# Performance work log

Hardware: AMD Instinct MI355X
Metric: run time of the kernel (lower is better)

The kernel has to match this reference:

```python
import jax, jax.numpy as jnp
import numpy as np
from jax import lax

B, S, I, H, NC = 64, 512, 512, 1024, 2


def _lstm_layer(x, w_ih, w_hh, b_ih, b_hh):
    """x: [B,S,Iin] -> hs: [B,S,H]. PyTorch gate order: i, f, g, o."""
    Bx = x.shape[0]
    Hh = w_hh.shape[1]
    b = b_ih + b_hh
    # Precompute input contribution for all timesteps: [S,B,4H]
    xg = jnp.einsum('bsi,gi->sbg', x, w_ih) + b

    def step(carry, xg_t):
        h, c = carry
        gates = xg_t + h @ w_hh.T  # [B,4H]
        i, f, g, o = jnp.split(gates, 4, axis=-1)
        i = jax.nn.sigmoid(i)
        f = jax.nn.sigmoid(f)
        g = jnp.tanh(g)
        o = jax.nn.sigmoid(o)
        c = f * c + i * g
        h = o * jnp.tanh(c)
        return (h, c), h

    h0 = jnp.zeros((Bx, Hh), x.dtype)
    c0 = jnp.zeros((Bx, Hh), x.dtype)
    (_, _), hs = lax.scan(step, (h0, c0), xg)
    return jnp.transpose(hs, (1, 0, 2))  # [B,S,H]


def setup_inputs() -> dict:
    key = jax.random.key(0)
    ks = jax.random.split(key, 11)
    s_i = 1.0 / np.sqrt(H)
    return {
        'x': jax.random.normal(ks[0], (B, S, I), jnp.float32),
        'w_ih0': jax.random.uniform(ks[1], (4 * H, I), jnp.float32, -s_i, s_i),
        'w_hh0': jax.random.uniform(ks[2], (4 * H, H), jnp.float32, -s_i, s_i),
        'b_ih0': jax.random.uniform(ks[3], (4 * H,), jnp.float32, -s_i, s_i),
        'b_hh0': jax.random.uniform(ks[4], (4 * H,), jnp.float32, -s_i, s_i),
        'w_ih1': jax.random.uniform(ks[5], (4 * H, H), jnp.float32, -s_i, s_i),
        'w_hh1': jax.random.uniform(ks[6], (4 * H, H), jnp.float32, -s_i, s_i),
        'b_ih1': jax.random.uniform(ks[7], (4 * H,), jnp.float32, -s_i, s_i),
        'b_hh1': jax.random.uniform(ks[8], (4 * H,), jnp.float32, -s_i, s_i),
        'fc_w': jax.random.uniform(ks[9], (NC, H), jnp.float32, -s_i, s_i),
        'fc_b': jax.random.uniform(ks[10], (NC,), jnp.float32, -s_i, s_i),
    }


def reference(x, w_ih0, w_hh0, b_ih0, b_hh0, w_ih1, w_hh1, b_ih1, b_hh1, fc_w, fc_b):
    # dropout p=0.0 -> identity (eval semantics)
    h = _lstm_layer(x, w_ih0, w_hh0, b_ih0, b_hh0)
    h = _lstm_layer(h, w_ih1, w_hh1, b_ih1, b_hh1)
    last = h[:, -1, :]  # [B,H]
    logits = last @ fc_w.T + fc_b  # [B,NC]
    return jax.nn.softmax(logits, axis=1)
```

## Files before the change

### kernel.cpp

```cpp
#include <hip/hip_runtime.h>

typedef __attribute__((ext_vector_type(8))) short short8;
typedef __attribute__((ext_vector_type(4))) float f32x4;
typedef __attribute__((ext_vector_type(2))) unsigned int u32x2;
typedef unsigned short u16;
typedef unsigned int u32;

#define XB_OFF 0ul
#define H0_OFF 33554432ul
#define H1_OFF 100794368ul
#define FL_OFF 168034304ul
#define FLAGS_LEN 32768ul

#define LDS_TOTAL 131072

__device__ __forceinline__ u16 f2bf(float f) {
  u32 u = __float_as_uint(f);
  return (u16)((u + 0x7fffu + ((u >> 16) & 1u)) >> 16);
}
__device__ __forceinline__ float bf2f(u16 s) { return __uint_as_float(((u32)s) << 16); }

__global__ __launch_bounds__(256) void prep_x(const float* __restrict__ x,
                                              u16* __restrict__ xb) {
  u32 stride = gridDim.x * blockDim.x;
  for (u32 e = blockIdx.x * blockDim.x + threadIdx.x; e < 16777216u; e += stride) {
    u32 i = e & 511u, b = (e >> 9) & 63u, t = e >> 15;
    xb[e] = f2bf(x[((size_t)b << 18) + ((size_t)t << 9) + i]);
  }
}

__global__ __launch_bounds__(256, 1) void lstm_persist(
    const u16* __restrict__ xb,
    const float* __restrict__ wih0, const float* __restrict__ whh0,
    const float* __restrict__ bih0, const float* __restrict__ bhh0,
    const float* __restrict__ wih1, const float* __restrict__ whh1,
    const float* __restrict__ bih1, const float* __restrict__ bhh1,
    u16* __restrict__ h0h, u16* __restrict__ h1h,
    u32* __restrict__ flags,
    const float* __restrict__ fc_w, const float* __restrict__ fc_b,
    float* __restrict__ out) {
  extern __shared__ char smem[];
  const int cu = blockIdx.x;
  const int layer = cu >> 7;
  const int lcu = cu & 127;
  const int U0 = lcu * 8;
  const int K2 = layer ? 4096 : 3072;
  const int tid = threadIdx.x;

  for (int n = 0; n < 32; ++n) {
    const int grow = (n >> 3) * 1024 + U0 + (n & 7);
    char* colbase = smem + n * K2;
    const u32 swn = (u32)(n & 7) << 4;
    if (!layer) {
      const float* rih = wih0 + (size_t)grow * 512;
      const float* rhh = whh0 + (size_t)grow * 1024;
      for (int k = tid; k < 1536; k += 256) {
        float v = (k < 512) ? rih[k] : rhh[k - 512];
        *(u16*)(colbase + (((u32)k * 2u) ^ swn)) = f2bf(v);
      }
    } else {
      const float* rih = wih1 + (size_t)grow * 1024;
      const float* rhh = whh1 + (size_t)grow * 1024;
      for (int k = tid; k < 2048; k += 256) {
        float v = (k < 1024) ? rih[k] : rhh[k - 1024];
        *(u16*)(colbase + (((u32)k * 2u) ^ swn)) = f2bf(v);
      }
    }
  }
  __syncthreads();

  const int g = tid >> 6;
  const int lane = tid & 63;
  const int lr = lane & 15;
  const int lq = lane >> 4;
  const u32 swz = (u32)(lr & 7) << 4;
  const char* wrow0 = smem + (size_t)lr * K2;
  const char* wrow1 = smem + (size_t)(16 + lr) * K2;

  float bi[4], bf_[4], bg[4], bo[4];
  {
    const float* s1 = layer ? bih1 : bih0;
    const float* s2 = layer ? bhh1 : bhh0;
    const int ug = U0 + 4 * (lq & 1);
    #pragma unroll
    for (int r = 0; r < 4; ++r) {
      bi[r]  = s1[ug + r]        + s2[ug + r];
      bf_[r] = s1[1024 + ug + r] + s2[1024 + ug + r];
      bg[r]  = s1[2048 + ug + r] + s2[2048 + ug + r];
      bo[r]  = s1[3072 + ug + r] + s2[3072 + ug + r];
    }
  }
  float cs[4] = {0.f, 0.f, 0.f, 0.f};

  const u32* f0g = flags + (size_t)(0 * 4 + g) * 1024;
  const u32* f1g = flags + (size_t)(1 * 4 + g) * 1024;
  u32* myflag = flags + ((size_t)(layer * 4 + g) * 128 + (size_t)lcu) * 8;

  auto poll2 = [&](const u32* base, u32 target) {
    const u32* p1 = base + (u32)lane * 8u;
    const u32* p2 = base + (u32)(lane + 64) * 8u;
    for (;;) {
      u32 v1, v2;
      asm volatile("global_load_dword %0, %2, off sc0 sc1\n\t"
                   "global_load_dword %1, %3, off sc0 sc1\n\t"
                   "s_waitcnt vmcnt(0)"
                   : "=v"(v1), "=v"(v2) : "v"(p1), "v"(p2) : "memory");
      if (__all((int)((v1 >= target) & (v2 >= target)))) break;
      __builtin_amdgcn_s_sleep(1);
    }
  };

  f32x4 z4 = {0.f, 0.f, 0.f, 0.f};
  f32x4 acc0, acc1;

  auto mfma2 = [&](short8 hb8, int k0) {
    const u32 kb = ((u32)(k0 + lq * 8) * 2u) ^ swz;
    short8 a0 = *(const short8*)(wrow0 + kb);
    short8 a1 = *(const short8*)(wrow1 + kb);
    acc0 = __builtin_amdgcn_mfma_f32_16x16x32_bf16(a0, hb8, acc0, 0, 0, 0);
    acc1 = __builtin_amdgcn_mfma_f32_16x16x32_bf16(a1, hb8, acc1, 0, 0, 0);
  };

  auto cell_publish = [&](int t, u16* hist) {
    float pf[4], po[4];
    #pragma unroll
    for (int r = 0; r < 4; ++r) {
      pf[r] = __shfl_xor(acc0[r], 32);
      po[r] = __shfl_xor(acc1[r], 32);
    }
    if (lq < 2) {
      u16 hb16[4];
      #pragma unroll
      for (int r = 0; r < 4; ++r) {
        float gi = acc0[r] + bi[r];
        float gf = pf[r]   + bf_[r];
        float gg = acc1[r] + bg[r];
        float go = po[r]   + bo[r];
        float ii = 1.0f / (1.0f + __expf(-gi));
        float ff = 1.0f / (1.0f + __expf(-gf));
        float gt = 1.0f - 2.0f / (__expf(2.0f * gg) + 1.0f);
        float oo = 1.0f / (1.0f + __expf(-go));
        cs[r] = ff * cs[r] + ii * gt;
        hb16[r] = f2bf(oo * (1.0f - 2.0f / (__expf(2.0f * cs[r]) + 1.0f)));
      }
      u32x2 pk;
      pk.x = (u32)hb16[0] | ((u32)hb16[1] << 16);
      pk.y = (u32)hb16[2] | ((u32)hb16[3] << 16);
      u16* dst = hist + (size_t)(t + 1) * 65536 + (size_t)g * 16384
                 + (size_t)lcu * 128 + (size_t)lr * 8 + 4 * lq;
      asm volatile("global_store_dwordx2 %0, %1, off sc0 sc1" :: "v"(dst), "v"(pk));
    }
    asm volatile("s_waitcnt vmcnt(0)" ::: "memory");
    if (lane == 0)
      asm volatile("global_store_dword %0, %1, off sc0 sc1"
                   :: "v"(myflag), "v"((u32)(t + 1)));
  };

  if (!layer) {
    for (int t = 0; t < 512; ++t) {
      acc0 = z4; acc1 = z4;
      const u16* xp = xb + (size_t)t * 32768 + (size_t)(g * 16 + lr) * 512 + lq * 8;
      short8 X[16];
      #pragma unroll
      for (int j = 0; j < 16; ++j) X[j] = *(const short8*)(xp + j * 32);
      #pragma unroll
      for (int j = 0; j < 16; ++j) mfma2(X[j], j * 32);
      if (t > 0) {
        poll2(f0g, (u32)t);
        const u16* hp = h0h + (size_t)t * 65536 + (size_t)g * 16384 + (size_t)lr * 8;
        short8 H[32];
        #pragma unroll
        for (int j = 0; j < 32; ++j)
          H[j] = *(const short8*)(hp + (size_t)(j * 4 + lq) * 128);
        #pragma unroll
        for (int j = 0; j < 32; ++j) mfma2(H[j], 512 + j * 32);
      }
      cell_publish(t, h0h);
    }
  } else {
    for (int t = 0; t < 512; ++t) {
      acc0 = z4; acc1 = z4;
      if (t > 0) {
        poll2(f1g, (u32)t);
        const u16* hp1 = h1h + (size_t)t * 65536 + (size_t)g * 16384 + (size_t)lr * 8;
        short8 H1[32];
        #pragma unroll
        for (int j = 0; j < 32; ++j)
          H1[j] = *(const short8*)(hp1 + (size_t)(j * 4 + lq) * 128);
        #pragma unroll
        for (int j = 0; j < 32; ++j) mfma2(H1[j], 1024 + j * 32);
      }
      poll2(f0g, (u32)(t + 1));
      const u16* hp0 = h0h + (size_t)(t + 1) * 65536 + (size_t)g * 16384 + (size_t)lr * 8;
      short8 H0[32];
      #pragma unroll
      for (int j = 0; j < 32; ++j)
        H0[j] = *(const short8*)(hp0 + (size_t)(j * 4 + lq) * 128);
      #pragma unroll
      for (int j = 0; j < 32; ++j) mfma2(H0[j], j * 32);
      cell_publish(t, h1h);
    }
  }

  if (cu == 0 && g == 0) {
    #pragma unroll
    for (int j = 0; j < 8; ++j) {
      const u32* p = flags + (size_t)(512 + j * 64 + lane) * 8;
      for (;;) {
        u32 v;
        asm volatile("global_load_dword %0, %1, off sc0 sc1\n\ts_waitcnt vmcnt(0)"
                     : "=v"(v) : "v"(p) : "memory");
        if (v >= 512u) break;
        __builtin_amdgcn_s_sleep(1);
      }
    }
    const int b = lane;
    const u16* hb = h1h + (size_t)512 * 65536 + (size_t)(b >> 4) * 16384
                    + (size_t)(b & 15) * 8;
    float s0 = fc_b[0], s1 = fc_b[1];
    for (int c = 0; c < 128; ++c) {
      short8 hv8 = *(const short8*)(hb + (size_t)c * 128);
      #pragma unroll
      for (int e = 0; e < 8; ++e) {
        float hv = bf2f((u16)hv8[e]);
        s0 += hv * fc_w[c * 8 + e];
        s1 += hv * fc_w[1024 + c * 8 + e];
      }
    }
    float mx = fmaxf(s0, s1);
    float e0 = __expf(s0 - mx), e1 = __expf(s1 - mx);
    float inv = 1.0f / (e0 + e1);
    out[b * 2]     = e0 * inv;
    out[b * 2 + 1] = e1 * inv;
  }
}

extern "C" void kernel_launch(void* const* d_in, const int* in_sizes, int n_in,
                              void* d_out, int out_size, void* d_ws, size_t ws_size,
                              hipStream_t stream) {
  const float* x    = (const float*)d_in[0];
  const float* wih0 = (const float*)d_in[1];
  const float* whh0 = (const float*)d_in[2];
  const float* bih0 = (const float*)d_in[3];
  const float* bhh0 = (const float*)d_in[4];
  const float* wih1 = (const float*)d_in[5];
  const float* whh1 = (const float*)d_in[6];
  const float* bih1 = (const float*)d_in[7];
  const float* bhh1 = (const float*)d_in[8];
  const float* fcw  = (const float*)d_in[9];
  const float* fcb  = (const float*)d_in[10];
  float* out = (float*)d_out;
  char* ws = (char*)d_ws;

  u16* xb    = (u16*)(ws + XB_OFF);
  u16* h0h   = (u16*)(ws + H0_OFF);
  u16* h1h   = (u16*)(ws + H1_OFF);
  u32* flags = (u32*)(ws + FL_OFF);

  (void)hipFuncSetAttribute((const void*)lstm_persist,
      hipFuncAttributeMaxDynamicSharedMemorySize, LDS_TOTAL);

  hipMemsetAsync(ws + FL_OFF, 0, FLAGS_LEN, stream);
  prep_x<<<8192, 256, 0, stream>>>(x, xb);
  lstm_persist<<<256, 256, LDS_TOTAL, stream>>>(
      (const u16*)xb, wih0, whh0, bih0, bhh0, wih1, whh1, bih1, bhh1,
      h0h, h1h, flags, fcw, fcb, out);
}
```

Measured before the change: 3.727 ms.

## Switch recurrent GEMM to 32x32x16 MFMA with two waves per block

Result: slower. 4.063 ms (+9.0%).

```diff
diff --git a/kernel.cpp b/kernel.cpp
--- a/kernel.cpp
+++ b/kernel.cpp
@@ -1,7 +1,7 @@
 #include <hip/hip_runtime.h>
 
 typedef __attribute__((ext_vector_type(8))) short short8;
-typedef __attribute__((ext_vector_type(4))) float f32x4;
+typedef __attribute__((ext_vector_type(16))) float f32x16;
 typedef __attribute__((ext_vector_type(2))) unsigned int u32x2;
 typedef unsigned short u16;
 typedef unsigned int u32;
@@ -10,9 +10,9 @@
 #define H0_OFF 33554432ul
 #define H1_OFF 100794368ul
 #define FL_OFF 168034304ul
-#define FLAGS_LEN 32768ul
-
-#define LDS_TOTAL 131072
+#define FLAGS_LEN 16384ul
+
+#define LDS_TOTAL 131584
 
 __device__ __forceinline__ u16 f2bf(float f) {
   u32 u = __float_as_uint(f);
@@ -24,12 +24,19 @@
                                               u16* __restrict__ xb) {
   u32 stride = gridDim.x * blockDim.x;
   for (u32 e = blockIdx.x * blockDim.x + threadIdx.x; e < 16777216u; e += stride) {
-    u32 i = e & 511u, b = (e >> 9) & 63u, t = e >> 15;
-    xb[e] = f2bf(x[((size_t)b << 18) + ((size_t)t << 9) + i]);
-  }
-}
-
-__global__ __launch_bounds__(256, 1) void lstm_persist(
+    u32 t = e >> 15;
+    u32 r = e & 32767u;
+    u32 w = r >> 14;
+    u32 r2 = r & 16383u;
+    u32 c = r2 >> 8;
+    u32 r3 = r2 & 255u;
+    u32 b = r3 >> 3, u = r3 & 7u;
+    u32 gb = w * 32u + b;
+    xb[e] = f2bf(x[(size_t)gb * 262144 + (size_t)t * 512 + c * 8 + u]);
+  }
+}
+
+__global__ __launch_bounds__(128, 1) void lstm_persist(
     const u16* __restrict__ xb,
     const float* __restrict__ wih0, const float* __restrict__ whh0,
     const float* __restrict__ bih0, const float* __restrict__ bhh0,
@@ -44,44 +51,37 @@
   const int layer = cu >> 7;
   const int lcu = cu & 127;
   const int U0 = lcu * 8;
-  const int K2 = layer ? 4096 : 3072;
+  const int K2P = layer ? (4096 + 16) : (3072 + 16);
   const int tid = threadIdx.x;
 
   for (int n = 0; n < 32; ++n) {
     const int grow = (n >> 3) * 1024 + U0 + (n & 7);
-    char* colbase = smem + n * K2;
-    const u32 swn = (u32)(n & 7) << 4;
+    u16* colbase = (u16*)(smem + n * K2P);
     if (!layer) {
       const float* rih = wih0 + (size_t)grow * 512;
       const float* rhh = whh0 + (size_t)grow * 1024;
-      for (int k = tid; k < 1536; k += 256) {
-        float v = (k < 512) ? rih[k] : rhh[k - 512];
-        *(u16*)(colbase + (((u32)k * 2u) ^ swn)) = f2bf(v);
-      }
+      for (int k = tid; k < 1536; k += 128)
+        colbase[k] = f2bf(k < 512 ? rih[k] : rhh[k - 512]);
     } else {
       const float* rih = wih1 + (size_t)grow * 1024;
       const float* rhh = whh1 + (size_t)grow * 1024;
-      for (int k = tid; k < 2048; k += 256) {
-        float v = (k < 1024) ? rih[k] : rhh[k - 1024];
-        *(u16*)(colbase + (((u32)k * 2u) ^ swn)) = f2bf(v);
-      }
+      for (int k = tid; k < 2048; k += 128)
+        colbase[k] = f2bf(k < 1024 ? rih[k] : rhh[k - 1024]);
     }
   }
   __syncthreads();
 
-  const int g = tid >> 6;
+  const int w = tid >> 6;
   const int lane = tid & 63;
-  const int lr = lane & 15;
-  const int lq = lane >> 4;
-  const u32 swz = (u32)(lr & 7) << 4;
-  const char* wrow0 = smem + (size_t)lr * K2;
-  const char* wrow1 = smem + (size_t)(16 + lr) * K2;
+  const int b = lane & 31;
+  const int hi = lane >> 5;
+  const char* wbase = smem + (size_t)(lane & 31) * K2P + hi * 16;
 
   float bi[4], bf_[4], bg[4], bo[4];
   {
     const float* s1 = layer ? bih1 : bih0;
     const float* s2 = layer ? bhh1 : bhh0;
-    const int ug = U0 + 4 * (lq & 1);
+    const int ug = U0 + 4 * hi;
     #pragma unroll
     for (int r = 0; r < 4; ++r) {
       bi[r]  = s1[ug + r]        + s2[ug + r];
@@ -92,11 +92,11 @@
   }
   float cs[4] = {0.f, 0.f, 0.f, 0.f};
 
-  const u32* f0g = flags + (size_t)(0 * 4 + g) * 1024;
-  const u32* f1g = flags + (size_t)(1 * 4 + g) * 1024;
-  u32* myflag = flags + ((size_t)(layer * 4 + g) * 128 + (size_t)lcu) * 8;
-
-  auto poll2 = [&](const u32* base, u32 target) {
+  const u32* f0w = flags + (size_t)(0 * 2 + w) * 128 * 8;
+  const u32* f1w = flags + (size_t)(1 * 2 + w) * 128 * 8;
+  u32* myflag = flags + ((size_t)(layer * 2 + w) * 128 + (size_t)lcu) * 8;
+
+  auto poll = [&](const u32* base, u32 target) {
     const u32* p1 = base + (u32)lane * 8u;
     const u32* p2 = base + (u32)(lane + 64) * 8u;
     for (;;) {
@@ -110,102 +110,118 @@
     }
   };
 
-  f32x4 z4 = {0.f, 0.f, 0.f, 0.f};
-  f32x4 acc0, acc1;
-
-  auto mfma2 = [&](short8 hb8, int k0) {
-    const u32 kb = ((u32)(k0 + lq * 8) * 2u) ^ swz;
-    short8 a0 = *(const short8*)(wrow0 + kb);
-    short8 a1 = *(const short8*)(wrow1 + kb);
-    acc0 = __builtin_amdgcn_mfma_f32_16x16x32_bf16(a0, hb8, acc0, 0, 0, 0);
-    acc1 = __builtin_amdgcn_mfma_f32_16x16x32_bf16(a1, hb8, acc1, 0, 0, 0);
-  };
-
-  auto cell_publish = [&](int t, u16* hist) {
-    float pf[4], po[4];
+  f32x16 acc[4];
+
+  auto publish = [&](int t, u16* hist) {
+    f32x16 s;
+    #pragma unroll
+    for (int r = 0; r < 16; ++r) s[r] = acc[0][r] + acc[1][r] + acc[2][r] + acc[3][r];
+    float hv[4];
     #pragma unroll
     for (int r = 0; r < 4; ++r) {
-      pf[r] = __shfl_xor(acc0[r], 32);
-      po[r] = __shfl_xor(acc1[r], 32);
-    }
-    if (lq < 2) {
-      u16 hb16[4];
-      #pragma unroll
-      for (int r = 0; r < 4; ++r) {
-        float gi = acc0[r] + bi[r];
-        float gf = pf[r]   + bf_[r];
-        float gg = acc1[r] + bg[r];
-        float go = po[r]   + bo[r];
-        float ii = 1.0f / (1.0f + __expf(-gi));
-        float ff = 1.0f / (1.0f + __expf(-gf));
-        float gt = 1.0f - 2.0f / (__expf(2.0f * gg) + 1.0f);
-        float oo = 1.0f / (1.0f + __expf(-go));
-        cs[r] = ff * cs[r] + ii * gt;
-        hb16[r] = f2bf(oo * (1.0f - 2.0f / (__expf(2.0f * cs[r]) + 1.0f)));
-      }
-      u32x2 pk;
-      pk.x = (u32)hb16[0] | ((u32)hb16[1] << 16);
-      pk.y = (u32)hb16[2] | ((u32)hb16[3] << 16);
-      u16* dst = hist + (size_t)(t + 1) * 65536 + (size_t)g * 16384
-                 + (size_t)lcu * 128 + (size_t)lr * 8 + 4 * lq;
-      asm volatile("global_store_dwordx2 %0, %1, off sc0 sc1" :: "v"(dst), "v"(pk));
-    }
+      float gi = s[r]      + bi[r];
+      float gf = s[4 + r]  + bf_[r];
+      float gg = s[8 + r]  + bg[r];
+      float go = s[12 + r] + bo[r];
+      float ii = 1.0f / (1.0f + __expf(-gi));
+      float ff = 1.0f / (1.0f + __expf(-gf));
+      float gt = 1.0f - 2.0f / (__expf(2.0f * gg) + 1.0f);
+      float oo = 1.0f / (1.0f + __expf(-go));
+      cs[r] = ff * cs[r] + ii * gt;
+      hv[r] = oo * (1.0f - 2.0f / (__expf(2.0f * cs[r]) + 1.0f));
+    }
+    u32x2 pk;
+    pk.x = (u32)f2bf(hv[0]) | ((u32)f2bf(hv[1]) << 16);
+    pk.y = (u32)f2bf(hv[2]) | ((u32)f2bf(hv[3]) << 16);
+    u16* dst = hist + (size_t)(t + 1) * 65536 + (size_t)w * 32768
+               + (size_t)lcu * 256 + (size_t)b * 8 + 4 * hi;
+    asm volatile("global_store_dwordx2 %0, %1, off sc0 sc1" :: "v"(dst), "v"(pk));
     asm volatile("s_waitcnt vmcnt(0)" ::: "memory");
     if (lane == 0)
       asm volatile("global_store_dword %0, %1, off sc0 sc1"
                    :: "v"(myflag), "v"((u32)(t + 1)));
   };
 
+  #define MFMA_T(buf, tile) do {                                            \
+    short8 _a = *(const short8*)(wbase + (tile) * 32);                      \
+    acc[(tile) & 3] = __builtin_amdgcn_mfma_f32_32x32x16_bf16(              \
+        _a, (buf), acc[(tile) & 3], 0, 0, 0);                               \
+  } while (0)
+
   if (!layer) {
     for (int t = 0; t < 512; ++t) {
-      acc0 = z4; acc1 = z4;
-      const u16* xp = xb + (size_t)t * 32768 + (size_t)(g * 16 + lr) * 512 + lq * 8;
-      short8 X[16];
-      #pragma unroll
-      for (int j = 0; j < 16; ++j) X[j] = *(const short8*)(xp + j * 32);
-      #pragma unroll
-      for (int j = 0; j < 16; ++j) mfma2(X[j], j * 32);
-      if (t > 0) {
-        poll2(f0g, (u32)t);
-        const u16* hp = h0h + (size_t)t * 65536 + (size_t)g * 16384 + (size_t)lr * 8;
-        short8 H[32];
-        #pragma unroll
-        for (int j = 0; j < 32; ++j)
-          H[j] = *(const short8*)(hp + (size_t)(j * 4 + lq) * 128);
-        #pragma unroll
-        for (int j = 0; j < 32; ++j) mfma2(H[j], 512 + j * 32);
-      }
-      cell_publish(t, h0h);
+      #pragma unroll
+      for (int a = 0; a < 4; ++a)
+        #pragma unroll
+        for (int r = 0; r < 16; ++r) acc[a][r] = 0.f;
+      short8 U[32], V[32];
+      const u16* xp = xb + (size_t)t * 32768 + (size_t)w * 16384
+                      + (size_t)hi * 256 + (size_t)b * 8;
+      #pragma unroll
+      for (int j = 0; j < 32; ++j) U[j] = *(const short8*)(xp + j * 512);
+      const u16* hp = h0h + (size_t)t * 65536 + (size_t)w * 32768
+                      + (size_t)hi * 256 + (size_t)b * 8;
+      if (t > 0) {
+        poll(f0w, (u32)t);
+        #pragma unroll
+        for (int j = 0; j < 32; ++j) V[j] = *(const short8*)(hp + j * 512);
+      }
+      #pragma unroll
+      for (int j = 0; j < 32; ++j) MFMA_T(U[j], j);
+      if (t > 0) {
+        #pragma unroll
+        for (int j = 0; j < 32; ++j) U[j] = *(const short8*)(hp + 16384 + j * 512);
+        #pragma unroll
+        for (int j = 0; j < 32; ++j) MFMA_T(V[j], 32 + j);
+        #pragma unroll
+        for (int j = 0; j < 32; ++j) MFMA_T(U[j], 64 + j);
+      }
+      publish(t, h0h);
     }
   } else {
     for (int t = 0; t < 512; ++t) {
-      acc0 = z4; acc1 = z4;
-      if (t > 0) {
-        poll2(f1g, (u32)t);
-        const u16* hp1 = h1h + (size_t)t * 65536 + (size_t)g * 16384 + (size_t)lr * 8;
-        short8 H1[32];
-        #pragma unroll
-        for (int j = 0; j < 32; ++j)
-          H1[j] = *(const short8*)(hp1 + (size_t)(j * 4 + lq) * 128);
-        #pragma unroll
-        for (int j = 0; j < 32; ++j) mfma2(H1[j], 1024 + j * 32);
-      }
-      poll2(f0g, (u32)(t + 1));
-      const u16* hp0 = h0h + (size_t)(t + 1) * 65536 + (size_t)g * 16384 + (size_t)lr * 8;
-      short8 H0[32];
-      #pragma unroll
-      for (int j = 0; j < 32; ++j)
-        H0[j] = *(const short8*)(hp0 + (size_t)(j * 4 + lq) * 128);
-      #pragma unroll
-      for (int j = 0; j < 32; ++j) mfma2(H0[j], j * 32);
-      cell_publish(t, h1h);
-    }
-  }
-
-  if (cu == 0 && g == 0) {
-    #pragma unroll
-    for (int j = 0; j < 8; ++j) {
-      const u32* p = flags + (size_t)(512 + j * 64 + lane) * 8;
+      #pragma unroll
+      for (int a = 0; a < 4; ++a)
+        #pragma unroll
+        for (int r = 0; r < 16; ++r) acc[a][r] = 0.f;
+      short8 U[32], V[32];
+      const u16* h1p = h1h + (size_t)t * 65536 + (size_t)w * 32768
+                       + (size_t)hi * 256 + (size_t)b * 8;
+      const u16* h0p = h0h + (size_t)(t + 1) * 65536 + (size_t)w * 32768
+                       + (size_t)hi * 256 + (size_t)b * 8;
+      if (t > 0) {
+        poll(f1w, (u32)t);
+        #pragma unroll
+        for (int j = 0; j < 32; ++j) U[j] = *(const short8*)(h1p + j * 512);
+      }
+      poll(f0w, (u32)(t + 1));
+      #pragma unroll
+      for (int j = 0; j < 32; ++j) V[j] = *(const short8*)(h0p + j * 512);
+      if (t > 0) {
+        #pragma unroll
+        for (int j = 0; j < 32; ++j) MFMA_T(U[j], 64 + j);
+        #pragma unroll
+        for (int j = 0; j < 32; ++j) U[j] = *(const short8*)(h1p + 16384 + j * 512);
+      }
+      #pragma unroll
+      for (int j = 0; j < 32; ++j) MFMA_T(V[j], j);
+      #pragma unroll
+      for (int j = 0; j < 32; ++j) V[j] = *(const short8*)(h0p + 16384 + j * 512);
+      if (t > 0) {
+        #pragma unroll
+        for (int j = 0; j < 32; ++j) MFMA_T(U[j], 96 + j);
+      }
+      #pragma unroll
+      for (int j = 0; j < 32; ++j) MFMA_T(V[j], 32 + j);
+      publish(t, h1h);
+    }
+  }
+  #undef MFMA_T
+
+  if (cu == 0 && tid < 64) {
+    #pragma unroll
+    for (int j = 0; j < 4; ++j) {
+      const u32* p = flags + (size_t)(256 + lane + 64 * j) * 8;
       for (;;) {
         u32 v;
         asm volatile("global_load_dword %0, %1, off sc0 sc1\n\ts_waitcnt vmcnt(0)"
@@ -214,12 +230,12 @@
         __builtin_amdgcn_s_sleep(1);
       }
     }
-    const int b = lane;
-    const u16* hb = h1h + (size_t)512 * 65536 + (size_t)(b >> 4) * 16384
-                    + (size_t)(b & 15) * 8;
+    const int bb = lane;
+    const u16* hb = h1h + (size_t)512 * 65536 + (size_t)(bb >> 5) * 32768
+                    + (size_t)(bb & 31) * 8;
     float s0 = fc_b[0], s1 = fc_b[1];
     for (int c = 0; c < 128; ++c) {
-      short8 hv8 = *(const short8*)(hb + (size_t)c * 128);
+      short8 hv8 = *(const short8*)(hb + (size_t)c * 256);
       #pragma unroll
       for (int e = 0; e < 8; ++e) {
         float hv = bf2f((u16)hv8[e]);
@@ -230,8 +246,8 @@
     float mx = fmaxf(s0, s1);
     float e0 = __expf(s0 - mx), e1 = __expf(s1 - mx);
     float inv = 1.0f / (e0 + e1);
-    out[b * 2]     = e0 * inv;
-    out[b * 2 + 1] = e1 * inv;
+    out[bb * 2]     = e0 * inv;
+    out[bb * 2 + 1] = e1 * inv;
   }
 }
 
@@ -262,7 +278,7 @@
 
   hipMemsetAsync(ws + FL_OFF, 0, FLAGS_LEN, stream);
   prep_x<<<8192, 256, 0, stream>>>(x, xb);
-  lstm_persist<<<256, 256, LDS_TOTAL, stream>>>(
+  lstm_persist<<<256, 128, LDS_TOTAL, stream>>>(
       (const u16*)xb, wih0, whh0, bih0, bhh0, wih1, whh1, bih1, bhh1,
       h0h, h1h, flags, fcw, fcb, out);
 }
```

## Overlap flag polling with h-store drain, pad LDS rows, reorder loads

Applied to the files above, without the earlier changes.

Result: slower. 5.130 ms (+37.6%).

```diff
diff --git a/kernel.cpp b/kernel.cpp
--- a/kernel.cpp
+++ b/kernel.cpp
@@ -12,7 +12,7 @@
 #define FL_OFF 168034304ul
 #define FLAGS_LEN 32768ul
 
-#define LDS_TOTAL 131072
+#define LDS_TOTAL 131584
 
 __device__ __forceinline__ u16 f2bf(float f) {
   u32 u = __float_as_uint(f);
@@ -44,27 +44,22 @@
   const int layer = cu >> 7;
   const int lcu = cu & 127;
   const int U0 = lcu * 8;
-  const int K2 = layer ? 4096 : 3072;
+  const int K2P = layer ? (4096 + 16) : (3072 + 16);
   const int tid = threadIdx.x;
 
   for (int n = 0; n < 32; ++n) {
     const int grow = (n >> 3) * 1024 + U0 + (n & 7);
-    char* colbase = smem + n * K2;
-    const u32 swn = (u32)(n & 7) << 4;
+    u16* colbase = (u16*)(smem + n * K2P);
     if (!layer) {
       const float* rih = wih0 + (size_t)grow * 512;
       const float* rhh = whh0 + (size_t)grow * 1024;
-      for (int k = tid; k < 1536; k += 256) {
-        float v = (k < 512) ? rih[k] : rhh[k - 512];
-        *(u16*)(colbase + (((u32)k * 2u) ^ swn)) = f2bf(v);
-      }
+      for (int k = tid; k < 1536; k += 256)
+        colbase[k] = f2bf(k < 512 ? rih[k] : rhh[k - 512]);
     } else {
       const float* rih = wih1 + (size_t)grow * 1024;
       const float* rhh = whh1 + (size_t)grow * 1024;
-      for (int k = tid; k < 2048; k += 256) {
-        float v = (k < 1024) ? rih[k] : rhh[k - 1024];
-        *(u16*)(colbase + (((u32)k * 2u) ^ swn)) = f2bf(v);
-      }
+      for (int k = tid; k < 2048; k += 256)
+        colbase[k] = f2bf(k < 1024 ? rih[k] : rhh[k - 1024]);
     }
   }
   __syncthreads();
@@ -73,9 +68,8 @@
   const int lane = tid & 63;
   const int lr = lane & 15;
   const int lq = lane >> 4;
-  const u32 swz = (u32)(lr & 7) << 4;
-  const char* wrow0 = smem + (size_t)lr * K2;
-  const char* wrow1 = smem + (size_t)(16 + lr) * K2;
+  const char* wrow0 = smem + (size_t)lr * K2P;
+  const char* wrow1 = smem + (size_t)(16 + lr) * K2P;
 
   float bi[4], bf_[4], bg[4], bo[4];
   {
@@ -93,35 +87,46 @@
   float cs[4] = {0.f, 0.f, 0.f, 0.f};
 
   const u32* f0g = flags + (size_t)(0 * 4 + g) * 1024;
-  const u32* f1g = flags + (size_t)(1 * 4 + g) * 1024;
+  const u32* f1g = flags + (size_t)(4 + g) * 1024;
   u32* myflag = flags + ((size_t)(layer * 4 + g) * 128 + (size_t)lcu) * 8;
 
-  auto poll2 = [&](const u32* base, u32 target) {
+  const u32 sm1 = (lcu < 64 && lane == lcu) ? 0xFFFFFFFFu : 0u;
+  const u32 sm2 = (lcu >= 64 && lane == lcu - 64) ? 0xFFFFFFFFu : 0u;
+
+  auto pv2 = [&](const u32* base, u32& a, u32& b) {
     const u32* p1 = base + (u32)lane * 8u;
     const u32* p2 = base + (u32)(lane + 64) * 8u;
-    for (;;) {
-      u32 v1, v2;
-      asm volatile("global_load_dword %0, %2, off sc0 sc1\n\t"
-                   "global_load_dword %1, %3, off sc0 sc1\n\t"
-                   "s_waitcnt vmcnt(0)"
-                   : "=v"(v1), "=v"(v2) : "v"(p1), "v"(p2) : "memory");
-      if (__all((int)((v1 >= target) & (v2 >= target)))) break;
-      __builtin_amdgcn_s_sleep(1);
-    }
+    asm volatile("global_load_dword %0, %2, off sc0 sc1\n\t"
+                 "global_load_dword %1, %3, off sc0 sc1\n\t"
+                 "s_waitcnt vmcnt(0)"
+                 : "=v"(a), "=v"(b) : "v"(p1), "v"(p2) : "memory");
+  };
+  auto pv4 = [&](u32& a, u32& b, u32& c, u32& d) {
+    const u32* p1 = f1g + (u32)lane * 8u;
+    const u32* p2 = f1g + (u32)(lane + 64) * 8u;
+    const u32* p3 = f0g + (u32)lane * 8u;
+    const u32* p4 = f0g + (u32)(lane + 64) * 8u;
+    asm volatile("global_load_dword %0, %4, off sc0 sc1\n\t"
+                 "global_load_dword %1, %5, off sc0 sc1\n\t"
+                 "global_load_dword %2, %6, off sc0 sc1\n\t"
+                 "global_load_dword %3, %7, off sc0 sc1\n\t"
+                 "s_waitcnt vmcnt(0)"
+                 : "=v"(a), "=v"(b), "=v"(c), "=v"(d)
+                 : "v"(p1), "v"(p2), "v"(p3), "v"(p4) : "memory");
   };
 
   f32x4 z4 = {0.f, 0.f, 0.f, 0.f};
   f32x4 acc0, acc1;
 
   auto mfma2 = [&](short8 hb8, int k0) {
-    const u32 kb = ((u32)(k0 + lq * 8) * 2u) ^ swz;
+    const u32 kb = (u32)(k0 + lq * 8) * 2u;
     short8 a0 = *(const short8*)(wrow0 + kb);
     short8 a1 = *(const short8*)(wrow1 + kb);
     acc0 = __builtin_amdgcn_mfma_f32_16x16x32_bf16(a0, hb8, acc0, 0, 0, 0);
     acc1 = __builtin_amdgcn_mfma_f32_16x16x32_bf16(a1, hb8, acc1, 0, 0, 0);
   };
 
-  auto cell_publish = [&](int t, u16* hist) {
+  auto cell_store = [&](int t, u16* hist) {
     float pf[4], po[4];
     #pragma unroll
     for (int r = 0; r < 4; ++r) {
@@ -150,55 +155,87 @@
                  + (size_t)lcu * 128 + (size_t)lr * 8 + 4 * lq;
       asm volatile("global_store_dwordx2 %0, %1, off sc0 sc1" :: "v"(dst), "v"(pk));
     }
-    asm volatile("s_waitcnt vmcnt(0)" ::: "memory");
+  };
+  auto flag_pub = [&](int t) {
     if (lane == 0)
       asm volatile("global_store_dword %0, %1, off sc0 sc1"
                    :: "v"(myflag), "v"((u32)(t + 1)));
   };
 
   if (!layer) {
+    u32 v1 = 0, v2 = 0;
     for (int t = 0; t < 512; ++t) {
       acc0 = z4; acc1 = z4;
       const u16* xp = xb + (size_t)t * 32768 + (size_t)(g * 16 + lr) * 512 + lq * 8;
       short8 X[16];
       #pragma unroll
       for (int j = 0; j < 16; ++j) X[j] = *(const short8*)(xp + j * 32);
-      #pragma unroll
-      for (int j = 0; j < 16; ++j) mfma2(X[j], j * 32);
       if (t > 0) {
-        poll2(f0g, (u32)t);
+        const u32 tt = (u32)t;
+        while (!__all((int)(((v1 | sm1) >= tt) & ((v2 | sm2) >= tt)))) {
+          __builtin_amdgcn_s_sleep(1);
+          pv2(f0g, v1, v2);
+        }
         const u16* hp = h0h + (size_t)t * 65536 + (size_t)g * 16384 + (size_t)lr * 8;
         short8 H[32];
         #pragma unroll
         for (int j = 0; j < 32; ++j)
           H[j] = *(const short8*)(hp + (size_t)(j * 4 + lq) * 128);
         #pragma unroll
+        for (int j = 0; j < 16; ++j) mfma2(X[j], j * 32);
+        #pragma unroll
         for (int j = 0; j < 32; ++j) mfma2(H[j], 512 + j * 32);
-      }
-      cell_publish(t, h0h);
+      } else {
+        #pragma unroll
+        for (int j = 0; j < 16; ++j) mfma2(X[j], j * 32);
+      }
+      cell_store(t, h0h);
+      pv2(f0g, v1, v2);
+      flag_pub(t);
     }
   } else {
+    u32 v1 = 0, v2 = 0, v3 = 0, v4 = 0;
     for (int t = 0; t < 512; ++t) {
       acc0 = z4; acc1 = z4;
       if (t > 0) {
-        poll2(f1g, (u32)t);
-        const u16* hp1 = h1h + (size_t)t * 65536 + (size_t)g * 16384 + (size_t)lr * 8;
-        short8 H1[32];
+        const u32 ta = (u32)t, tb = (u32)(t + 1);
+        while (!__all((int)(((v1 | sm1) >= ta) & ((v2 | sm2) >= ta) &
+                            (v3 >= tb) & (v4 >= tb)))) {
+          __builtin_amdgcn_s_sleep(1);
+          pv4(v1, v2, v3, v4);
+        }
+        const u16* h1p = h1h + (size_t)t * 65536 + (size_t)g * 16384 + (size_t)lr * 8;
+        const u16* h0p = h0h + (size_t)(t + 1) * 65536 + (size_t)g * 16384 + (size_t)lr * 8;
+        short8 A[32], Bv[32];
         #pragma unroll
         for (int j = 0; j < 32; ++j)
-          H1[j] = *(const short8*)(hp1 + (size_t)(j * 4 + lq) * 128);
-        #pragma unroll
-        for (int j = 0; j < 32; ++j) mfma2(H1[j], 1024 + j * 32);
-      }
-      poll2(f0g, (u32)(t + 1));
-      const u16* hp0 = h0h + (size_t)(t + 1) * 65536 + (size_t)g * 16384 + (size_t)lr * 8;
-      short8 H0[32];
-      #pragma unroll
-      for (int j = 0; j < 32; ++j)
-        H0[j] = *(const short8*)(hp0 + (size_t)(j * 4 + lq) * 128);
-      #pragma unroll
-      for (int j = 0; j < 32; ++j) mfma2(H0[j], j * 32);
-      cell_publish(t, h1h);
+          A[j] = *(const short8*)(h1p + (size_t)(j * 4 + lq) * 128);
+        #pragma unroll
+        for (int j = 0; j < 16; ++j)
+          Bv[j] = *(const short8*)(h0p + (size_t)(j * 4 + lq) * 128);
+        #pragma unroll
+        for (int j = 0; j < 32; ++j) mfma2(A[j], 1024 + j * 32);
+        #pragma unroll
+        for (int j = 16; j < 32; ++j)
+          Bv[j] = *(const short8*)(h0p + (size_t)(j * 4 + lq) * 128);
+        #pragma unroll
+        for (int j = 0; j < 32; ++j) mfma2(Bv[j], j * 32);
+      } else {
+        while (!__all((int)((v3 >= 1u) & (v4 >= 1u)))) {
+          __builtin_amdgcn_s_sleep(1);
+          pv4(v1, v2, v3, v4);
+        }
+        const u16* h0p = h0h + (size_t)65536 + (size_t)g * 16384 + (size_t)lr * 8;
+        short8 Bv[32];
+        #pragma unroll
+        for (int j = 0; j < 32; ++j)
+          Bv[j] = *(const short8*)(h0p + (size_t)(j * 4 + lq) * 128);
+        #pragma unroll
+        for (int j = 0; j < 32; ++j) mfma2(Bv[j], j * 32);
+      }
+      cell_store(t, h1h);
+      pv4(v1, v2, v3, v4);
+      flag_pub(t);
     }
   }
 
```

## Run both LSTM layers in every block with a wavefront-skewed pipeline

Applied to the files above, without the earlier changes.

Result: slower. 7.711 ms (+106.9%).

```diff
diff --git a/kernel.cpp b/kernel.cpp
--- a/kernel.cpp
+++ b/kernel.cpp
@@ -2,7 +2,6 @@
 
 typedef __attribute__((ext_vector_type(8))) short short8;
 typedef __attribute__((ext_vector_type(4))) float f32x4;
-typedef __attribute__((ext_vector_type(2))) unsigned int u32x2;
 typedef unsigned short u16;
 typedef unsigned int u32;
 
@@ -10,9 +9,12 @@
 #define H0_OFF 33554432ul
 #define H1_OFF 100794368ul
 #define FL_OFF 168034304ul
-#define FLAGS_LEN 32768ul
-
-#define LDS_TOTAL 131072
+#define FLAGS_LEN 65536ul
+
+#define S0B 3108
+#define S1B 4132
+#define L1OFF 49728
+#define LDS_TOTAL 115840
 
 __device__ __forceinline__ u16 f2bf(float f) {
   u32 u = __float_as_uint(f);
@@ -41,171 +43,159 @@
     float* __restrict__ out) {
   extern __shared__ char smem[];
   const int cu = blockIdx.x;
-  const int layer = cu >> 7;
-  const int lcu = cu & 127;
-  const int U0 = lcu * 8;
-  const int K2 = layer ? 4096 : 3072;
+  const int U0 = cu * 4;
   const int tid = threadIdx.x;
 
-  for (int n = 0; n < 32; ++n) {
-    const int grow = (n >> 3) * 1024 + U0 + (n & 7);
-    char* colbase = smem + n * K2;
-    const u32 swn = (u32)(n & 7) << 4;
-    if (!layer) {
-      const float* rih = wih0 + (size_t)grow * 512;
-      const float* rhh = whh0 + (size_t)grow * 1024;
-      for (int k = tid; k < 1536; k += 256) {
-        float v = (k < 512) ? rih[k] : rhh[k - 512];
-        *(u16*)(colbase + (((u32)k * 2u) ^ swn)) = f2bf(v);
-      }
-    } else {
-      const float* rih = wih1 + (size_t)grow * 1024;
-      const float* rhh = whh1 + (size_t)grow * 1024;
-      for (int k = tid; k < 2048; k += 256) {
-        float v = (k < 1024) ? rih[k] : rhh[k - 1024];
-        *(u16*)(colbase + (((u32)k * 2u) ^ swn)) = f2bf(v);
-      }
-    }
+  for (int n = 0; n < 16; ++n) {
+    const int grow = (n & 3) * 1024 + U0 + (n >> 2);
+    u16* c0 = (u16*)(smem + n * S0B);
+    const float* rih = wih0 + (size_t)grow * 512;
+    const float* rhh = whh0 + (size_t)grow * 1024;
+    for (int k = tid; k < 1536; k += 256)
+      c0[k] = f2bf(k < 512 ? rih[k] : rhh[k - 512]);
+    u16* c1 = (u16*)(smem + L1OFF + n * S1B);
+    const float* qih = wih1 + (size_t)grow * 1024;
+    const float* qhh = whh1 + (size_t)grow * 1024;
+    for (int k = tid; k < 2048; k += 256)
+      c1[k] = f2bf(k < 1024 ? qih[k] : qhh[k - 1024]);
   }
   __syncthreads();
 
-  const int g = tid >> 6;
-  const int lane = tid & 63;
-  const int lr = lane & 15;
-  const int lq = lane >> 4;
-  const u32 swz = (u32)(lr & 7) << 4;
-  const char* wrow0 = smem + (size_t)lr * K2;
-  const char* wrow1 = smem + (size_t)(16 + lr) * K2;
-
-  float bi[4], bf_[4], bg[4], bo[4];
+  const int g = tid >> 6, lane = tid & 63, lr = lane & 15, lq = lane >> 4;
+  const char* a0base = smem + (size_t)lr * S0B + lq * 16;
+  const char* a1base = smem + L1OFF + (size_t)lr * S1B + lq * 16;
+
+  float b0v[4], b1v[4];
+  #pragma unroll
+  for (int r = 0; r < 4; ++r) {
+    b0v[r] = bih0[r * 1024 + U0 + lq] + bhh0[r * 1024 + U0 + lq];
+    b1v[r] = bih1[r * 1024 + U0 + lq] + bhh1[r * 1024 + U0 + lq];
+  }
+  float c0s = 0.f, c1s = 0.f;
+
+  u32* fl0 = flags;
+  u32* fl1 = flags + 4 * 256 * 8;
+  const u32* f0g = fl0 + (size_t)g * 2048;
+  const u32* f1g = fl1 + (size_t)g * 2048;
+  u32* myf0 = fl0 + ((size_t)g * 256 + cu) * 8;
+  u32* myf1 = fl1 + ((size_t)g * 256 + cu) * 8;
+
+  const size_t pidx = (size_t)g * 16384 + (size_t)lr * 1024 + (U0 + lq);
+  const size_t cidx = (size_t)g * 16384 + (size_t)lr * 1024 + 8 * lq;
+
+  short8 X[16], H0[32], H1[32];
   {
-    const float* s1 = layer ? bih1 : bih0;
-    const float* s2 = layer ? bhh1 : bhh0;
-    const int ug = U0 + 4 * (lq & 1);
+    const u16* xp = xb + (size_t)(g * 16 + lr) * 512 + 8 * lq;
     #pragma unroll
-    for (int r = 0; r < 4; ++r) {
-      bi[r]  = s1[ug + r]        + s2[ug + r];
-      bf_[r] = s1[1024 + ug + r] + s2[1024 + ug + r];
-      bg[r]  = s1[2048 + ug + r] + s2[2048 + ug + r];
-      bo[r]  = s1[3072 + ug + r] + s2[3072 + ug + r];
-    }
-  }
-  float cs[4] = {0.f, 0.f, 0.f, 0.f};
-
-  const u32* f0g = flags + (size_t)(0 * 4 + g) * 1024;
-  const u32* f1g = flags + (size_t)(1 * 4 + g) * 1024;
-  u32* myflag = flags + ((size_t)(layer * 4 + g) * 128 + (size_t)lcu) * 8;
-
-  auto poll2 = [&](const u32* base, u32 target) {
-    const u32* p1 = base + (u32)lane * 8u;
-    const u32* p2 = base + (u32)(lane + 64) * 8u;
-    for (;;) {
-      u32 v1, v2;
-      asm volatile("global_load_dword %0, %2, off sc0 sc1\n\t"
-                   "global_load_dword %1, %3, off sc0 sc1\n\t"
-                   "s_waitcnt vmcnt(0)"
-                   : "=v"(v1), "=v"(v2) : "v"(p1), "v"(p2) : "memory");
-      if (__all((int)((v1 >= target) & (v2 >= target)))) break;
-      __builtin_amdgcn_s_sleep(1);
-    }
-  };
-
-  f32x4 z4 = {0.f, 0.f, 0.f, 0.f};
-  f32x4 acc0, acc1;
-
-  auto mfma2 = [&](short8 hb8, int k0) {
-    const u32 kb = ((u32)(k0 + lq * 8) * 2u) ^ swz;
-    short8 a0 = *(const short8*)(wrow0 + kb);
-    short8 a1 = *(const short8*)(wrow1 + kb);
-    acc0 = __builtin_amdgcn_mfma_f32_16x16x32_bf16(a0, hb8, acc0, 0, 0, 0);
-    acc1 = __builtin_amdgcn_mfma_f32_16x16x32_bf16(a1, hb8, acc1, 0, 0, 0);
-  };
-
-  auto cell_publish = [&](int t, u16* hist) {
-    float pf[4], po[4];
-    #pragma unroll
-    for (int r = 0; r < 4; ++r) {
-      pf[r] = __shfl_xor(acc0[r], 32);
-      po[r] = __shfl_xor(acc1[r], 32);
-    }
-    if (lq < 2) {
-      u16 hb16[4];
-      #pragma unroll
-      for (int r = 0; r < 4; ++r) {
-        float gi = acc0[r] + bi[r];
-        float gf = pf[r]   + bf_[r];
-        float gg = acc1[r] + bg[r];
-        float go = po[r]   + bo[r];
-        float ii = 1.0f / (1.0f + __expf(-gi));
-        float ff = 1.0f / (1.0f + __expf(-gf));
-        float gt = 1.0f - 2.0f / (__expf(2.0f * gg) + 1.0f);
-        float oo = 1.0f / (1.0f + __expf(-go));
-        cs[r] = ff * cs[r] + ii * gt;
-        hb16[r] = f2bf(oo * (1.0f - 2.0f / (__expf(2.0f * cs[r]) + 1.0f)));
-      }
-      u32x2 pk;
-      pk.x = (u32)hb16[0] | ((u32)hb16[1] << 16);
-      pk.y = (u32)hb16[2] | ((u32)hb16[3] << 16);
-      u16* dst = hist + (size_t)(t + 1) * 65536 + (size_t)g * 16384
-                 + (size_t)lcu * 128 + (size_t)lr * 8 + 4 * lq;
-      asm volatile("global_store_dwordx2 %0, %1, off sc0 sc1" :: "v"(dst), "v"(pk));
-    }
-    asm volatile("s_waitcnt vmcnt(0)" ::: "memory");
-    if (lane == 0)
-      asm volatile("global_store_dword %0, %1, off sc0 sc1"
-                   :: "v"(myflag), "v"((u32)(t + 1)));
-  };
-
-  if (!layer) {
-    for (int t = 0; t < 512; ++t) {
-      acc0 = z4; acc1 = z4;
-      const u16* xp = xb + (size_t)t * 32768 + (size_t)(g * 16 + lr) * 512 + lq * 8;
-      short8 X[16];
-      #pragma unroll
-      for (int j = 0; j < 16; ++j) X[j] = *(const short8*)(xp + j * 32);
-      #pragma unroll
-      for (int j = 0; j < 16; ++j) mfma2(X[j], j * 32);
+    for (int j = 0; j < 16; ++j) X[j] = *(const short8*)(xp + j * 32);
+  }
+
+  for (int t = 0; t <= 512; ++t) {
+    if (t < 512) {
+      f32x4 acc = {0.f, 0.f, 0.f, 0.f};
+      #pragma unroll
+      for (int j = 0; j < 16; ++j) {
+        short8 a = *(const short8*)(a0base + j * 64);
+        acc = __builtin_amdgcn_mfma_f32_16x16x32_bf16(a, X[j], acc, 0, 0, 0);
+      }
       if (t > 0) {
-        poll2(f0g, (u32)t);
-        const u16* hp = h0h + (size_t)t * 65536 + (size_t)g * 16384 + (size_t)lr * 8;
-        short8 H[32];
-        #pragma unroll
-        for (int j = 0; j < 32; ++j)
-          H[j] = *(const short8*)(hp + (size_t)(j * 4 + lq) * 128);
-        #pragma unroll
-        for (int j = 0; j < 32; ++j) mfma2(H[j], 512 + j * 32);
-      }
-      cell_publish(t, h0h);
-    }
-  } else {
-    for (int t = 0; t < 512; ++t) {
-      acc0 = z4; acc1 = z4;
-      if (t > 0) {
-        poll2(f1g, (u32)t);
-        const u16* hp1 = h1h + (size_t)t * 65536 + (size_t)g * 16384 + (size_t)lr * 8;
-        short8 H1[32];
-        #pragma unroll
-        for (int j = 0; j < 32; ++j)
-          H1[j] = *(const short8*)(hp1 + (size_t)(j * 4 + lq) * 128);
-        #pragma unroll
-        for (int j = 0; j < 32; ++j) mfma2(H1[j], 1024 + j * 32);
-      }
-      poll2(f0g, (u32)(t + 1));
-      const u16* hp0 = h0h + (size_t)(t + 1) * 65536 + (size_t)g * 16384 + (size_t)lr * 8;
-      short8 H0[32];
-      #pragma unroll
-      for (int j = 0; j < 32; ++j)
-        H0[j] = *(const short8*)(hp0 + (size_t)(j * 4 + lq) * 128);
-      #pragma unroll
-      for (int j = 0; j < 32; ++j) mfma2(H0[j], j * 32);
-      cell_publish(t, h1h);
+        #pragma unroll
+        for (int j = 0; j < 32; ++j) {
+          short8 a = *(const short8*)(a0base + (16 + j) * 64);
+          acc = __builtin_amdgcn_mfma_f32_16x16x32_bf16(a, H0[j], acc, 0, 0, 0);
+        }
+      }
+      float gi = acc[0] + b0v[0], gf = acc[1] + b0v[1];
+      float gg = acc[2] + b0v[2], go = acc[3] + b0v[3];
+      float ii = 1.f / (1.f + __expf(-gi));
+      float ff = 1.f / (1.f + __expf(-gf));
+      float gt = 1.f - 2.f / (__expf(2.f * gg) + 1.f);
+      float oo = 1.f / (1.f + __expf(-go));
+      c0s = ff * c0s + ii * gt;
+      u32 hv = (u32)f2bf(oo * (1.f - 2.f / (__expf(2.f * c0s) + 1.f)));
+      u16* dst = h0h + (size_t)(t + 1) * 65536 + pidx;
+      asm volatile("global_store_short %0, %1, off sc0 sc1" :: "v"(dst), "v"(hv) : "memory");
+      asm volatile("s_waitcnt vmcnt(0)" ::: "memory");
+      if (lane == 0)
+        asm volatile("global_store_dword %0, %1, off sc0 sc1"
+                     :: "v"(myf0), "v"((u32)(t + 1)) : "memory");
+    }
+    if (t > 0) {
+      {
+        const u16* hp = h1h + (size_t)(t - 1) * 65536 + cidx;
+        #pragma unroll
+        for (int j = 0; j < 32; ++j) H1[j] = *(const short8*)(hp + j * 32);
+      }
+      f32x4 acc = {0.f, 0.f, 0.f, 0.f};
+      #pragma unroll
+      for (int j = 0; j < 32; ++j) {
+        short8 a = *(const short8*)(a1base + j * 64);
+        acc = __builtin_amdgcn_mfma_f32_16x16x32_bf16(a, H0[j], acc, 0, 0, 0);
+      }
+      #pragma unroll
+      for (int j = 0; j < 32; ++j) {
+        short8 a = *(const short8*)(a1base + (32 + j) * 64);
+        acc = __builtin_amdgcn_mfma_f32_16x16x32_bf16(a, H1[j], acc, 0, 0, 0);
+      }
+      float gi = acc[0] + b1v[0], gf = acc[1] + b1v[1];
+      float gg = acc[2] + b1v[2], go = acc[3] + b1v[3];
+      float ii = 1.f / (1.f + __expf(-gi));
+      float ff = 1.f / (1.f + __expf(-gf));
+      float gt = 1.f - 2.f / (__expf(2.f * gg) + 1.f);
+      float oo = 1.f / (1.f + __expf(-go));
+      c1s = ff * c1s + ii * gt;
+      u32 hv = (u32)f2bf(oo * (1.f - 2.f / (__expf(2.f * c1s) + 1.f)));
+      u16* dst = h1h + (size_t)t * 65536 + pidx;
+      asm volatile("global_store_short %0, %1, off sc0 sc1" :: "v"(dst), "v"(hv) : "memory");
+      asm volatile("s_waitcnt vmcnt(0)" ::: "memory");
+      if (lane == 0)
+        asm volatile("global_store_dword %0, %1, off sc0 sc1"
+                     :: "v"(myf1), "v"((u32)t) : "memory");
+    }
+    if (t < 512) {
+      {
+        const int tx = (t + 1 < 512) ? t + 1 : 511;
+        const u16* xp = xb + (size_t)tx * 32768 + (size_t)(g * 16 + lr) * 512 + 8 * lq;
+        #pragma unroll
+        for (int j = 0; j < 16; ++j) X[j] = *(const short8*)(xp + j * 32);
+      }
+      const u32 T0 = (u32)(t + 1), T1 = (u32)t;
+      const u32* p0 = f0g + (u32)lane * 8u;
+      const u32* q0 = f1g + (u32)lane * 8u;
+      for (;;) {
+        u32 a0, a1, a2, a3, e0, e1, e2, e3;
+        asm volatile(
+            "global_load_dword %0, %8, off sc0 sc1\n\t"
+            "global_load_dword %1, %9, off sc0 sc1\n\t"
+            "global_load_dword %2, %10, off sc0 sc1\n\t"
+            "global_load_dword %3, %11, off sc0 sc1\n\t"
+            "global_load_dword %4, %12, off sc0 sc1\n\t"
+            "global_load_dword %5, %13, off sc0 sc1\n\t"
+            "global_load_dword %6, %14, off sc0 sc1\n\t"
+            "global_load_dword %7, %15, off sc0 sc1\n\t"
+            "s_waitcnt vmcnt(0)"
+            : "=v"(a0), "=v"(a1), "=v"(a2), "=v"(a3),
+              "=v"(e0), "=v"(e1), "=v"(e2), "=v"(e3)
+            : "v"(p0), "v"(p0 + 512), "v"(p0 + 1024), "v"(p0 + 1536),
+              "v"(q0), "v"(q0 + 512), "v"(q0 + 1024), "v"(q0 + 1536)
+            : "memory");
+        if (__all((int)((a0 >= T0) & (a1 >= T0) & (a2 >= T0) & (a3 >= T0) &
+                        (e0 >= T1) & (e1 >= T1) & (e2 >= T1) & (e3 >= T1))))
+          break;
+        __builtin_amdgcn_s_sleep(1);
+      }
+      {
+        const u16* hp = h0h + (size_t)(t + 1) * 65536 + cidx;
+        #pragma unroll
+        for (int j = 0; j < 32; ++j) H0[j] = *(const short8*)(hp + j * 32);
+      }
     }
   }
 
   if (cu == 0 && g == 0) {
     #pragma unroll
-    for (int j = 0; j < 8; ++j) {
-      const u32* p = flags + (size_t)(512 + j * 64 + lane) * 8;
+    for (int j = 0; j < 16; ++j) {
+      const u32* p = (flags + 4 * 256 * 8) + (size_t)(j * 64 + lane) * 8;
       for (;;) {
         u32 v;
         asm volatile("global_load_dword %0, %1, off sc0 sc1\n\ts_waitcnt vmcnt(0)"
@@ -216,10 +206,10 @@
     }
     const int b = lane;
     const u16* hb = h1h + (size_t)512 * 65536 + (size_t)(b >> 4) * 16384
-                    + (size_t)(b & 15) * 8;
+                    + (size_t)(b & 15) * 1024;
     float s0 = fc_b[0], s1 = fc_b[1];
     for (int c = 0; c < 128; ++c) {
-      short8 hv8 = *(const short8*)(hb + (size_t)c * 128);
+      short8 hv8 = *(const short8*)(hb + c * 8);
       #pragma unroll
       for (int e = 0; e < 8; ++e) {
         float hv = bf2f((u16)hv8[e]);
@@ -229,7 +219,7 @@
     }
     float mx = fmaxf(s0, s1);
     float e0 = __expf(s0 - mx), e1 = __expf(s1 - mx);
-    float inv = 1.0f / (e0 + e1);
+    float inv = 1.f / (e0 + e1);
     out[b * 2]     = e0 * inv;
     out[b * 2 + 1] = e1 * inv;
   }
@@ -261,6 +251,8 @@
       hipFuncAttributeMaxDynamicSharedMemorySize, LDS_TOTAL);
 
   hipMemsetAsync(ws + FL_OFF, 0, FLAGS_LEN, stream);
+  hipMemsetAsync(ws + H0_OFF, 0, 131072, stream);
+  hipMemsetAsync(ws + H1_OFF, 0, 131072, stream);
   prep_x<<<8192, 256, 0, stream>>>(x, xb);
   lstm_persist<<<256, 256, LDS_TOTAL, stream>>>(
       (const u16*)xb, wih0, whh0, bih0, bhh0, wih1, whh1, bih1, bhh1,
```
